# Optimization experiments

Measured on AMD Instinct MI355X. Metric: run time of the kernel, lower is better.

## Reference

```python
import jax, jax.numpy as jnp
import numpy as np

EMBED = 1024
HEADS = 16
HEAD_DIM = EMBED // HEADS
B, L = 4, 2048


def setup_inputs() -> dict:
    key = jax.random.key(0)
    ks = jax.random.split(key, 10)
    s = 1.0 / np.sqrt(EMBED)
    x = jax.random.normal(ks[0], (B, L, EMBED), dtype=jnp.float32)
    mask = jax.random.randint(ks[1], (B, 1, L, L), 0, 2, dtype=jnp.int32)
    Wq = jax.random.normal(ks[2], (EMBED, EMBED), dtype=jnp.float32) * s
    Wk = jax.random.normal(ks[3], (EMBED, EMBED), dtype=jnp.float32) * s
    Wv = jax.random.normal(ks[4], (EMBED, EMBED), dtype=jnp.float32) * s
    Wo = jax.random.normal(ks[5], (EMBED, EMBED), dtype=jnp.float32) * s
    bq = jnp.zeros((EMBED,), jnp.float32)
    bk = jnp.zeros((EMBED,), jnp.float32)
    bv = jnp.zeros((EMBED,), jnp.float32)
    bo = jnp.zeros((EMBED,), jnp.float32)
    return {"x": x, "mask": mask, "Wq": Wq, "bq": bq, "Wk": Wk, "bk": bk,
            "Wv": Wv, "bv": bv, "Wo": Wo, "bo": bo}


def reference(x, mask, Wq, bq, Wk, bk, Wv, bv, Wo, bo):
    n, l, _ = x.shape
    q = (x @ Wq + bq).reshape(n, l, HEADS, HEAD_DIM)
    k = (x @ Wk + bk).reshape(n, l, HEADS, HEAD_DIM)
    v = (x @ Wv + bv).reshape(n, l, HEADS, HEAD_DIM)
    # [n, h, q, k] scores
    energy = jnp.einsum('nqhd,nkhd->nhqk', q, k)
    energy = jnp.where(mask == 0, jnp.float32(-1e20), energy)
    attn = jax.nn.softmax(energy / jnp.sqrt(jnp.float32(HEAD_DIM)), axis=-1)
    out = jnp.einsum('nhqk,nkhd->nqhd', attn, v).reshape(n, l, EMBED)
    return out @ Wo + bo
```

## Files before the change

### kernel.cpp

```cpp
#include <hip/hip_runtime.h>
#include <hip/hip_bf16.h>

#define EMBED 1024
#define HEADS 16
#define HDIM 64
#define BATCH 4
#define SEQ 2048
#define ROWS (BATCH * SEQ)
#define LOG2E 1.4426950408889634f

typedef __attribute__((ext_vector_type(8))) short bf16x8;
typedef __attribute__((ext_vector_type(4))) float f32x4;

#define MFMA16(a, b, c) __builtin_amdgcn_mfma_f32_16x16x32_bf16(a, b, c, 0, 0, 0)

__device__ __forceinline__ unsigned short f2bf(float f) {
    union { float f; unsigned int u; } x; x.f = f;
    unsigned int r = x.u + 0x7fffu + ((x.u >> 16) & 1u);
    return (unsigned short)(r >> 16);
}

__device__ __forceinline__ unsigned int pkbf(float a, float b) {
#if __has_builtin(__builtin_amdgcn_cvt_pk_bf16_f32)
    auto v = __builtin_amdgcn_cvt_pk_bf16_f32(a, b);
    unsigned int u; __builtin_memcpy(&u, &v, 4); return u;
#else
    union { __hip_bfloat162 h; unsigned int u; } c;
    c.h = __float22bfloat162_rn(make_float2(a, b)); return c.u;
#endif
}

__device__ __forceinline__ void gl2lds(const unsigned short* g, unsigned short* l) {
    __builtin_amdgcn_global_load_lds(
        (const __attribute__((address_space(1))) unsigned int*)g,
        (__attribute__((address_space(3))) unsigned int*)l, 16, 0, 0);
}

#define XBLK 8192
#define MBLK 16384
#define WBLK 4096

__global__ __launch_bounds__(256) void prep_kernel(
    const float* __restrict__ x, const int* __restrict__ mask,
    const float* __restrict__ W0, const float* __restrict__ W1,
    const float* __restrict__ W2, const float* __restrict__ W3,
    unsigned short* __restrict__ Xb, unsigned char* __restrict__ m8,
    unsigned short* __restrict__ Wt)
{
    __shared__ float t[32][33];
    const int bid = blockIdx.x;
    if (bid < XBLK) {
        int i = (bid * 256 + threadIdx.x) * 4;
        float4 v = *(const float4*)(x + i);
        uint2 o; o.x = pkbf(v.x, v.y); o.y = pkbf(v.z, v.w);
        *(uint2*)(Xb + i) = o;
    } else if (bid < XBLK + MBLK) {
        int i = ((bid - XBLK) * 256 + threadIdx.x) * 4;
        int4 v = *(const int4*)(mask + i);
        uchar4 o;
        o.x = v.x ? 0xFF : 0; o.y = v.y ? 0xFF : 0;
        o.z = v.z ? 0xFF : 0; o.w = v.w ? 0xFF : 0;
        *(uchar4*)(m8 + i) = o;
    } else {
        int f = bid - XBLK - MBLK;
        int z = f >> 10, rem = f & 1023;
        const float* W = (z == 0) ? W0 : (z == 1) ? W1 : (z == 2) ? W2 : W3;
        unsigned short* o = Wt + (size_t)z * EMBED * EMBED;
        int tx = threadIdx.x & 31, ty = threadIdx.x >> 5;
        int bx = (rem & 31) * 32, by = (rem >> 5) * 32;
#pragma unroll
        for (int r = 0; r < 32; r += 8)
            t[ty + r][tx] = W[(size_t)(by + ty + r) * EMBED + bx + tx];
        __syncthreads();
#pragma unroll
        for (int r = 0; r < 32; r += 8)
            o[(size_t)(bx + ty + r) * EMBED + by + tx] = f2bf(t[tx][ty + r]);
    }
}

__device__ __forceinline__ void gemm_bf16_body(
    const unsigned short* __restrict__ A, const unsigned short* __restrict__ Bt,
    const float* __restrict__ bias,
    float* __restrict__ outF, unsigned short* __restrict__ outB, float scale,
    int vmode, int m0, int n0)
{
    __shared__ unsigned short As[128][64];
    __shared__ unsigned short Bs[128][64];
    const int tid = threadIdx.x;
    const int lane = tid & 63, wid = tid >> 6;
    const int ln = lane & 15, lg = lane >> 4;
    const int wy = wid >> 1, wx = wid & 1;
    const int r0 = wid * 32 + (lane >> 3);
    const int scol = (((lane & 7) ^ ((lane >> 3) & 7)) << 3);
    const unsigned short* Ap = A + (size_t)(m0 + r0) * EMBED + scol;
    const unsigned short* Bp = Bt + (size_t)(n0 + r0) * EMBED + scol;
    unsigned short* lA = &As[wid * 32][0];
    unsigned short* lB = &Bs[wid * 32][0];

    f32x4 acc[4][4];
#pragma unroll
    for (int i = 0; i < 4; i++)
#pragma unroll
        for (int j = 0; j < 4; j++) acc[i][j] = (f32x4){0.f, 0.f, 0.f, 0.f};

    for (int k0 = 0; k0 < EMBED; k0 += 64) {
        __syncthreads();
#pragma unroll
        for (int is = 0; is < 4; is++) {
            gl2lds(Ap + k0 + (size_t)(is * 8) * EMBED, lA + is * 8 * 64);
            gl2lds(Bp + k0 + (size_t)(is * 8) * EMBED, lB + is * 8 * 64);
        }
        __syncthreads();
        bf16x8 af[2][4], bfr[2][4];
#pragma unroll
        for (int s = 0; s < 2; s++) {
#pragma unroll
            for (int mi = 0; mi < 4; mi++)
                af[s][mi] = *(const bf16x8*)
                    &As[wy * 64 + mi * 16 + ln][(((lg + 4 * s) ^ (ln & 7)) << 3)];
#pragma unroll
            for (int nj = 0; nj < 4; nj++)
                bfr[s][nj] = *(const bf16x8*)
                    &Bs[wx * 64 + nj * 16 + ln][(((lg + 4 * s) ^ (ln & 7)) << 3)];
        }
#pragma unroll
        for (int s = 0; s < 2; s++)
#pragma unroll
            for (int mi = 0; mi < 4; mi++)
#pragma unroll
                for (int nj = 0; nj < 4; nj++)
                    acc[mi][nj] = MFMA16(af[s][mi], bfr[s][nj], acc[mi][nj]);
    }

#pragma unroll
    for (int mi = 0; mi < 4; mi++) {
#pragma unroll
        for (int nj = 0; nj < 4; nj++) {
            int row = m0 + wy * 64 + mi * 16 + lg * 4;
            int col = n0 + wx * 64 + nj * 16 + ln;
            float bv = bias[col];
            if (vmode) {
                int bb = row >> 11, s = row & (SEQ - 1);
                int hh = col >> 6, dd = col & 63;
                unsigned short* dst = outB +
                    ((size_t)((bb * HEADS + hh) * HDIM + dd)) * SEQ + s;
                uint2 pw;
                pw.x = pkbf(acc[mi][nj][0] + bv, acc[mi][nj][1] + bv);
                pw.y = pkbf(acc[mi][nj][2] + bv, acc[mi][nj][3] + bv);
                *(uint2*)dst = pw;
            } else {
#pragma unroll
                for (int r = 0; r < 4; r++) {
                    float v = (acc[mi][nj][r] + bv) * scale;
                    if (outF) outF[(size_t)(row + r) * EMBED + col] = v;
                    else      outB[(size_t)(row + r) * EMBED + col] = f2bf(v);
                }
            }
        }
    }
}

__global__ __launch_bounds__(256) void qkv_gemm_kernel(
    const unsigned short* __restrict__ Xb, const unsigned short* __restrict__ Wt,
    const float* __restrict__ bq, const float* __restrict__ bk,
    const float* __restrict__ bv,
    unsigned short* __restrict__ Qb, unsigned short* __restrict__ Kb,
    unsigned short* __restrict__ Vt)
{
    const int bid = blockIdx.x;
    const int xcd = bid & 7;
    const int idx = bid >> 3;
    const int bx  = idx & 7;
    const int yi  = (idx >> 3) & 7;
    const int z   = idx >> 6;
    const int by  = xcd * 8 + yi;

    const unsigned short* Bt = Wt + (size_t)z * EMBED * EMBED;
    const float* bias = (z == 0) ? bq : (z == 1) ? bk : bv;
    unsigned short* out = (z == 0) ? Qb : (z == 1) ? Kb : Vt;
    float scale = (z == 0) ? 0.125f * LOG2E : 1.0f;
    gemm_bf16_body(Xb, Bt, bias, nullptr, out, scale, z == 2,
                   by * 128, bx * 128);
}

__global__ __launch_bounds__(256) void out_gemm_kernel(
    const unsigned short* __restrict__ Ob, const unsigned short* __restrict__ Wto,
    const float* __restrict__ bo, float* __restrict__ out)
{
    const int bid = blockIdx.x;
    const int xcd = bid & 7;
    const int idx = bid >> 3;
    const int bx  = idx & 7;
    const int yi  = idx >> 3;
    const int by  = xcd * 8 + yi;
    gemm_bf16_body(Ob, Wto, bo, out, nullptr, 1.0f, 0, by * 128, bx * 128);
}

__global__ __launch_bounds__(256) void attn_mfma_kernel(
    const unsigned short* __restrict__ Qb, const unsigned short* __restrict__ Kb,
    const unsigned short* __restrict__ Vt, const unsigned char* __restrict__ mask8,
    unsigned short* __restrict__ Ob)
{
    __shared__ unsigned short Ks[64][64];
    __shared__ unsigned short Vs[64][64];
    const int tid = threadIdx.x;
    const int lane = tid & 63, wid = tid >> 6;
    const int ln = lane & 15, lg = lane >> 4;

    const int bid = blockIdx.x;
    const int xcd = bid & 7;
    const int i5 = bid >> 3;
    const int qx = i5 & 15;
    const int bh = xcd * 8 + (i5 >> 4);
    const int h = bh & 15, b = bh >> 4;
    const int q0 = qx * 128 + wid * 32;

    bf16x8 qf[2][2];
#pragma unroll
    for (int mi = 0; mi < 2; mi++)
#pragma unroll
        for (int ks = 0; ks < 2; ks++)
            qf[mi][ks] = *(const bf16x8*)(Qb +
                (size_t)(b * SEQ + q0 + mi * 16 + ln) * EMBED + h * HDIM + ks * 32 + lg * 8);

    bf16x8 ones;
#pragma unroll
    for (int i = 0; i < 8; i++) ones[i] = (short)0x3F80;

    f32x4 o[2][4];
#pragma unroll
    for (int mi = 0; mi < 2; mi++)
#pragma unroll
        for (int dj = 0; dj < 4; dj++) o[mi][dj] = (f32x4){0.f, 0.f, 0.f, 0.f};
    f32x4 lacc[2] = {(f32x4){0.f, 0.f, 0.f, 0.f}, (f32x4){0.f, 0.f, 0.f, 0.f}};

    const int srow = tid >> 3;
    const int scolK = (((tid & 7) ^ ((tid >> 3) & 7)) << 3);
    const unsigned short* Kp = Kb + (size_t)(b * SEQ + srow) * EMBED + h * HDIM + scolK;
    unsigned short* lK = &Ks[srow & ~7][0];

    const int vrow = tid >> 2, vu = tid & 3;
    const unsigned short* Vp = Vt + (size_t)((b * HEADS + h) * HDIM + vrow) * SEQ + 4 * vu;
    unsigned short* vdst = &Vs[vrow][0];
    const int vw0 = ((vu ^ (vrow & 7)) << 3);
    const int vw1 = (((vu + 4) ^ (vrow & 7)) << 3);

    const unsigned char* mq0 = mask8 + (size_t)b * SEQ * SEQ + (size_t)(q0 + ln) * SEQ;
    const unsigned char* mq1 = mq0 + (size_t)16 * SEQ;

    const int swk = ((lg ^ (ln & 7)) << 3);
    int vrd[2];
#pragma unroll
    for (int ks = 0; ks < 2; ks++)
        vrd[ks] = ((4 * ks + lg) ^ (ln & 7)) << 3;

    union U8 { bf16x8 v; unsigned int w[4]; };

    for (int kt = 0; kt < SEQ; kt += 64) {
        unsigned int mw[2][4];
#pragma unroll
        for (int mi = 0; mi < 2; mi++) {
            const unsigned char* mq = (mi ? mq1 : mq0) + kt;
#pragma unroll
            for (int nj = 0; nj < 4; nj++)
                mw[mi][nj] = *(const unsigned int*)(mq + nj * 16 + lg * 4);
        }

        uint2 v0 = *(const uint2*)(Vp + kt);
        uint2 v1 = *(const uint2*)(Vp + kt + 16);
        uint2 v2 = *(const uint2*)(Vp + kt + 32);
        uint2 v3 = *(const uint2*)(Vp + kt + 48);

        __syncthreads();
        gl2lds(Kp + (size_t)kt * EMBED, lK);
        gl2lds(Kp + (size_t)(kt + 32) * EMBED, lK + 32 * 64);
        {
            uint4 w0; w0.x = v0.x; w0.y = v0.y; w0.z = v1.x; w0.w = v1.y;
            uint4 w1; w1.x = v2.x; w1.y = v2.y; w1.z = v3.x; w1.w = v3.y;
            *(uint4*)(vdst + vw0) = w0;
            *(uint4*)(vdst + vw1) = w1;
        }
        __syncthreads();

        f32x4 S[2][4];
#pragma unroll
        for (int nj = 0; nj < 4; nj++) {
            bf16x8 k0 = *(const bf16x8*)&Ks[nj * 16 + ln][swk];
            bf16x8 k1 = *(const bf16x8*)&Ks[nj * 16 + ln][swk ^ 32];
#pragma unroll
            for (int mi = 0; mi < 2; mi++) {
                f32x4 t2 = (f32x4){0.f, 0.f, 0.f, 0.f};
                t2 = MFMA16(k0, qf[mi][0], t2);
                t2 = MFMA16(k1, qf[mi][1], t2);
                S[mi][nj] = t2;
            }
        }

        U8 pf[2][2];
#pragma unroll
        for (int mi = 0; mi < 2; mi++)
#pragma unroll
            for (int ks = 0; ks < 2; ks++)
#pragma unroll
                for (int hf = 0; hf < 2; hf++) {
                    const int nj = 2 * ks + hf;
                    float p0 = __builtin_amdgcn_exp2f(S[mi][nj][0]);
                    float p1 = __builtin_amdgcn_exp2f(S[mi][nj][1]);
                    float p2 = __builtin_amdgcn_exp2f(S[mi][nj][2]);
                    float p3 = __builtin_amdgcn_exp2f(S[mi][nj][3]);
                    unsigned int m = mw[mi][nj];
                    unsigned int d0 = __builtin_amdgcn_perm(0u, m, 0x01010000u);
                    unsigned int d1 = __builtin_amdgcn_perm(0u, m, 0x03030202u);
                    pf[mi][ks].w[2 * hf]     = pkbf(p0, p1) & d0;
                    pf[mi][ks].w[2 * hf + 1] = pkbf(p2, p3) & d1;
                }

#pragma unroll
        for (int ks = 0; ks < 2; ks++) {
            bf16x8 p0 = pf[0][ks].v;
            bf16x8 p1 = pf[1][ks].v;
            lacc[0] = MFMA16(p0, ones, lacc[0]);
            lacc[1] = MFMA16(p1, ones, lacc[1]);
#pragma unroll
            for (int dj = 0; dj < 4; dj++) {
                bf16x8 vf = *(const bf16x8*)&Vs[dj * 16 + ln][vrd[ks]];
                o[0][dj] = MFMA16(p0, vf, o[0][dj]);
                o[1][dj] = MFMA16(p1, vf, o[1][dj]);
            }
        }
    }

#pragma unroll
    for (int mi = 0; mi < 2; mi++) {
        float l0 = 1.0f / lacc[mi][0];
        float l1 = 1.0f / lacc[mi][1];
        float l2 = 1.0f / lacc[mi][2];
        float l3 = 1.0f / lacc[mi][3];
#pragma unroll
        for (int dj = 0; dj < 4; dj++) {
            unsigned short* op = Ob + (size_t)(b * SEQ + q0 + mi * 16 + lg * 4) * EMBED
                                    + h * HDIM + dj * 16 + ln;
            op[0]         = f2bf(o[mi][dj][0] * l0);
            op[EMBED]     = f2bf(o[mi][dj][1] * l1);
            op[2 * EMBED] = f2bf(o[mi][dj][2] * l2);
            op[3 * EMBED] = f2bf(o[mi][dj][3] * l3);
        }
    }
}

extern "C" void kernel_launch(void* const* d_in, const int* in_sizes, int n_in,
                              void* d_out, int out_size, void* d_ws, size_t ws_size,
                              hipStream_t stream)
{
    const float* x  = (const float*)d_in[0];
    const int* mask = (const int*)d_in[1];
    const float* Wq = (const float*)d_in[2];
    const float* bq = (const float*)d_in[3];
    const float* Wk = (const float*)d_in[4];
    const float* bk = (const float*)d_in[5];
    const float* Wv = (const float*)d_in[6];
    const float* bv = (const float*)d_in[7];
    const float* Wo = (const float*)d_in[8];
    const float* bo = (const float*)d_in[9];
    float* outp = (float*)d_out;

    char* ws = (char*)d_ws;
    unsigned short* Wt = (unsigned short*)(ws);
    unsigned char*  m8 = (unsigned char*)(ws + ((size_t)8 << 20));
    unsigned short* Xb = (unsigned short*)(ws + ((size_t)24 << 20));
    unsigned short* Ob = Xb;
    unsigned short* Qb = (unsigned short*)(ws + ((size_t)40 << 20));
    unsigned short* Kb = (unsigned short*)(ws + ((size_t)56 << 20));
    unsigned short* Vt = (unsigned short*)(ws + ((size_t)72 << 20));

    prep_kernel<<<XBLK + MBLK + WBLK, 256, 0, stream>>>(
        x, mask, Wq, Wk, Wv, Wo, Xb, m8, Wt);
    qkv_gemm_kernel<<<1536, 256, 0, stream>>>(
        Xb, Wt, bq, bk, bv, Qb, Kb, Vt);
    attn_mfma_kernel<<<1024, 256, 0, stream>>>(
        Qb, Kb, Vt, m8, Ob);
    out_gemm_kernel<<<512, 256, 0, stream>>>(
        Ob, Wt + (size_t)3 * EMBED * EMBED, bo, outp);
}
```

Measured before the change: 380.9 us.

## Double-buffer K/V tiles and mask in attention kernel to overlap loads with MFMA

Splits the K and V shared-memory tiles into two ping-pong buffers and issues the next tile's K global-to-LDS copy, V register loads and mask loads before computing on the current tile. Sched barriers pin the load issue ahead of the MFMA/exp work, and V is written to LDS afterwards. This cuts the syncs per tile from two to one and hides global latency behind compute. The cost is double the LDS footprint and more live registers, which may lower occupancy, plus one redundant wrap-around prefetch on the last iteration.

```diff
diff --git a/kernel.cpp b/kernel.cpp
--- a/kernel.cpp
+++ b/kernel.cpp
@@ -201,8 +201,8 @@
     const unsigned short* __restrict__ Vt, const unsigned char* __restrict__ mask8,
     unsigned short* __restrict__ Ob)
 {
-    __shared__ unsigned short Ks[64][64];
-    __shared__ unsigned short Vs[64][64];
+    __shared__ unsigned short Ks0[64][64], Ks1[64][64];
+    __shared__ unsigned short Vs0[64][64], Vs1[64][64];
     const int tid = threadIdx.x;
     const int lane = tid & 63, wid = tid >> 6;
     const int ln = lane & 15, lg = lane >> 4;
@@ -237,11 +237,11 @@
     const int srow = tid >> 3;
     const int scolK = (((tid & 7) ^ ((tid >> 3) & 7)) << 3);
     const unsigned short* Kp = Kb + (size_t)(b * SEQ + srow) * EMBED + h * HDIM + scolK;
-    unsigned short* lK = &Ks[srow & ~7][0];
+    const int lKo = (srow & ~7) * 64;
 
     const int vrow = tid >> 2, vu = tid & 3;
     const unsigned short* Vp = Vt + (size_t)((b * HEADS + h) * HDIM + vrow) * SEQ + 4 * vu;
-    unsigned short* vdst = &Vs[vrow][0];
+    const int vVo = vrow * 64;
     const int vw0 = ((vu ^ (vrow & 7)) << 3);
     const int vw1 = (((vu + 4) ^ (vrow & 7)) << 3);
 
@@ -255,80 +255,103 @@
         vrd[ks] = ((4 * ks + lg) ^ (ln & 7)) << 3;
 
     union U8 { bf16x8 v; unsigned int w[4]; };
-
-    for (int kt = 0; kt < SEQ; kt += 64) {
-        unsigned int mw[2][4];
-#pragma unroll
-        for (int mi = 0; mi < 2; mi++) {
-            const unsigned char* mq = (mi ? mq1 : mq0) + kt;
-#pragma unroll
-            for (int nj = 0; nj < 4; nj++)
-                mw[mi][nj] = *(const unsigned int*)(mq + nj * 16 + lg * 4);
-        }
-
-        uint2 v0 = *(const uint2*)(Vp + kt);
-        uint2 v1 = *(const uint2*)(Vp + kt + 16);
-        uint2 v2 = *(const uint2*)(Vp + kt + 32);
-        uint2 v3 = *(const uint2*)(Vp + kt + 48);
-
-        __syncthreads();
-        gl2lds(Kp + (size_t)kt * EMBED, lK);
-        gl2lds(Kp + (size_t)(kt + 32) * EMBED, lK + 32 * 64);
-        {
-            uint4 w0; w0.x = v0.x; w0.y = v0.y; w0.z = v1.x; w0.w = v1.y;
-            uint4 w1; w1.x = v2.x; w1.y = v2.y; w1.z = v3.x; w1.w = v3.y;
-            *(uint4*)(vdst + vw0) = w0;
-            *(uint4*)(vdst + vw1) = w1;
-        }
-        __syncthreads();
-
-        f32x4 S[2][4];
-#pragma unroll
-        for (int nj = 0; nj < 4; nj++) {
-            bf16x8 k0 = *(const bf16x8*)&Ks[nj * 16 + ln][swk];
-            bf16x8 k1 = *(const bf16x8*)&Ks[nj * 16 + ln][swk ^ 32];
-#pragma unroll
-            for (int mi = 0; mi < 2; mi++) {
-                f32x4 t2 = (f32x4){0.f, 0.f, 0.f, 0.f};
-                t2 = MFMA16(k0, qf[mi][0], t2);
-                t2 = MFMA16(k1, qf[mi][1], t2);
-                S[mi][nj] = t2;
-            }
-        }
-
-        U8 pf[2][2];
-#pragma unroll
-        for (int mi = 0; mi < 2; mi++)
-#pragma unroll
-            for (int ks = 0; ks < 2; ks++)
-#pragma unroll
-                for (int hf = 0; hf < 2; hf++) {
-                    const int nj = 2 * ks + hf;
-                    float p0 = __builtin_amdgcn_exp2f(S[mi][nj][0]);
-                    float p1 = __builtin_amdgcn_exp2f(S[mi][nj][1]);
-                    float p2 = __builtin_amdgcn_exp2f(S[mi][nj][2]);
-                    float p3 = __builtin_amdgcn_exp2f(S[mi][nj][3]);
-                    unsigned int m = mw[mi][nj];
-                    unsigned int d0 = __builtin_amdgcn_perm(0u, m, 0x01010000u);
-                    unsigned int d1 = __builtin_amdgcn_perm(0u, m, 0x03030202u);
-                    pf[mi][ks].w[2 * hf]     = pkbf(p0, p1) & d0;
-                    pf[mi][ks].w[2 * hf + 1] = pkbf(p2, p3) & d1;
-                }
-
-#pragma unroll
-        for (int ks = 0; ks < 2; ks++) {
-            bf16x8 p0 = pf[0][ks].v;
-            bf16x8 p1 = pf[1][ks].v;
-            lacc[0] = MFMA16(p0, ones, lacc[0]);
-            lacc[1] = MFMA16(p1, ones, lacc[1]);
-#pragma unroll
-            for (int dj = 0; dj < 4; dj++) {
-                bf16x8 vf = *(const bf16x8*)&Vs[dj * 16 + ln][vrd[ks]];
-                o[0][dj] = MFMA16(p0, vf, o[0][dj]);
-                o[1][dj] = MFMA16(p1, vf, o[1][dj]);
-            }
-        }
-    }
+    unsigned int mwA[2][4], mwB[2][4];
+
+    gl2lds(Kp, &Ks0[0][0] + lKo);
+    gl2lds(Kp + (size_t)32 * EMBED, &Ks0[0][0] + lKo + 32 * 64);
+    {
+        uint2 v0 = *(const uint2*)(Vp);
+        uint2 v1 = *(const uint2*)(Vp + 16);
+        uint2 v2 = *(const uint2*)(Vp + 32);
+        uint2 v3 = *(const uint2*)(Vp + 48);
+        uint4 w0; w0.x = v0.x; w0.y = v0.y; w0.z = v1.x; w0.w = v1.y;
+        uint4 w1; w1.x = v2.x; w1.y = v2.y; w1.z = v3.x; w1.w = v3.y;
+        *(uint4*)(&Vs0[0][0] + vVo + vw0) = w0;
+        *(uint4*)(&Vs0[0][0] + vVo + vw1) = w1;
+    }
+#pragma unroll
+    for (int mi = 0; mi < 2; mi++) {
+        const unsigned char* mq = mi ? mq1 : mq0;
+#pragma unroll
+        for (int nj = 0; nj < 4; nj++)
+            mwA[mi][nj] = *(const unsigned int*)(mq + nj * 16 + lg * 4);
+    }
+    __syncthreads();
+
+#define ATTN_ITER(KC, VC, KN, VN, MWC, MWN, NXT)                              \
+    {                                                                          \
+        const int nxt_ = (NXT);                                                \
+        gl2lds(Kp + (size_t)nxt_ * EMBED, &KN[0][0] + lKo);                    \
+        gl2lds(Kp + (size_t)(nxt_ + 32) * EMBED, &KN[0][0] + lKo + 32 * 64);   \
+        uint2 v0 = *(const uint2*)(Vp + nxt_);                                 \
+        uint2 v1 = *(const uint2*)(Vp + nxt_ + 16);                            \
+        uint2 v2 = *(const uint2*)(Vp + nxt_ + 32);                            \
+        uint2 v3 = *(const uint2*)(Vp + nxt_ + 48);                            \
+        _Pragma("unroll")                                                      \
+        for (int mi = 0; mi < 2; mi++) {                                       \
+            const unsigned char* mq = (mi ? mq1 : mq0) + nxt_;                 \
+            _Pragma("unroll")                                                  \
+            for (int nj = 0; nj < 4; nj++)                                     \
+                MWN[mi][nj] = *(const unsigned int*)(mq + nj * 16 + lg * 4);   \
+        }                                                                      \
+        __builtin_amdgcn_sched_barrier(0);  \
+        f32x4 S[2][4];                                                         \
+        _Pragma("unroll")                                                      \
+        for (int nj = 0; nj < 4; nj++) {                                       \
+            bf16x8 k0 = *(const bf16x8*)&KC[nj * 16 + ln][swk];                \
+            bf16x8 k1 = *(const bf16x8*)&KC[nj * 16 + ln][swk ^ 32];           \
+            _Pragma("unroll")                                                  \
+            for (int mi = 0; mi < 2; mi++) {                                   \
+                f32x4 t2 = (f32x4){0.f, 0.f, 0.f, 0.f};                        \
+                t2 = MFMA16(k0, qf[mi][0], t2);                                \
+                t2 = MFMA16(k1, qf[mi][1], t2);                                \
+                S[mi][nj] = t2;                                                \
+            }                                                                  \
+        }                                                                      \
+        U8 pf[2][2];                                                           \
+        _Pragma("unroll")                                                      \
+        for (int mi = 0; mi < 2; mi++)                                         \
+            _Pragma("unroll")                                                  \
+            for (int ks = 0; ks < 2; ks++)                                     \
+                _Pragma("unroll")                                              \
+                for (int hf = 0; hf < 2; hf++) {                               \
+                    const int nj = 2 * ks + hf;                                \
+                    float p0 = __builtin_amdgcn_exp2f(S[mi][nj][0]);           \
+                    float p1 = __builtin_amdgcn_exp2f(S[mi][nj][1]);           \
+                    float p2 = __builtin_amdgcn_exp2f(S[mi][nj][2]);           \
+                    float p3 = __builtin_amdgcn_exp2f(S[mi][nj][3]);           \
+                    unsigned int m = MWC[mi][nj];                              \
+                    unsigned int d0 = __builtin_amdgcn_perm(0u, m, 0x01010000u); \
+                    unsigned int d1 = __builtin_amdgcn_perm(0u, m, 0x03030202u); \
+                    pf[mi][ks].w[2 * hf]     = pkbf(p0, p1) & d0;              \
+                    pf[mi][ks].w[2 * hf + 1] = pkbf(p2, p3) & d1;              \
+                }                                                              \
+        _Pragma("unroll")                                                      \
+        for (int ks = 0; ks < 2; ks++) {                                       \
+            bf16x8 p0 = pf[0][ks].v;                                           \
+            bf16x8 p1 = pf[1][ks].v;                                           \
+            lacc[0] = MFMA16(p0, ones, lacc[0]);                               \
+            lacc[1] = MFMA16(p1, ones, lacc[1]);                               \
+            _Pragma("unroll")                                                  \
+            for (int dj = 0; dj < 4; dj++) {                                   \
+                bf16x8 vf = *(const bf16x8*)&VC[dj * 16 + ln][vrd[ks]];        \
+                o[0][dj] = MFMA16(p0, vf, o[0][dj]);                           \
+                o[1][dj] = MFMA16(p1, vf, o[1][dj]);                           \
+            }                                                                  \
+        }                                                                      \
+        __builtin_amdgcn_sched_barrier(0);  \
+        uint4 w0; w0.x = v0.x; w0.y = v0.y; w0.z = v1.x; w0.w = v1.y;          \
+        uint4 w1; w1.x = v2.x; w1.y = v2.y; w1.z = v3.x; w1.w = v3.y;          \
+        *(uint4*)(&VN[0][0] + vVo + vw0) = w0;                                 \
+        *(uint4*)(&VN[0][0] + vVo + vw1) = w1;                                 \
+        __syncthreads();                                                       \
+    }
+
+    for (int kt = 0; kt < SEQ; kt += 128) {
+        ATTN_ITER(Ks0, Vs0, Ks1, Vs1, mwA, mwB, kt + 64)
+        ATTN_ITER(Ks1, Vs1, Ks0, Vs0, mwB, mwA, (kt + 128) & (SEQ - 1))
+    }
+#undef ATTN_ITER
 
 #pragma unroll
     for (int mi = 0; mi < 2; mi++) {
```

Measured after the change: 393.1 us. 1.03x slower.
